# Kernel tuning notes

Hardware: AMD Instinct MI355X
Metric: run time of the kernel (lower is better)

## Reference

```python
import jax, jax.numpy as jnp
import numpy as np

B, NPG, DEG, D, OUT = 256, 256, 16, 128, 12  # graphs, nodes/graph, avg degree, width, out dim
N = B * NPG
E = N * DEG
K = NPG // 2  # TopKPooling ratio 0.5
BN_EPS = 1e-5


def setup_inputs() -> dict:
    key = jax.random.key(0)
    ks = jax.random.split(key, 12)
    x = jax.random.randint(ks[0], (N, 9), 0, 128)
    # within-graph random edges
    local = jax.random.randint(ks[1], (2, B, NPG * DEG), 0, NPG)
    edge_index = (local + (jnp.arange(B) * NPG)[None, :, None]).reshape(2, E)
    edge_attr = jax.random.randint(ks[2], (E, 3), 0, 16)
    batch = jnp.repeat(jnp.arange(B), NPG)
    return {
        "x": x,
        "edge_index": edge_index,
        "edge_attr": edge_attr,
        "batch": batch,
        "atom_emb": jax.random.normal(ks[3], (9, 128, D), jnp.float32) * 0.1,
        "bond_emb": jax.random.normal(ks[4], (3, 16, D), jnp.float32) * 0.1,
        "conv_W": jax.random.normal(ks[5], (5, D, D), jnp.float32) * 0.05,
        "conv_b": jnp.zeros((5, D), jnp.float32),
        "bn_gamma": jnp.ones((5, D), jnp.float32),
        "bn_beta": jnp.zeros((5, D), jnp.float32),
        "eps": jnp.zeros((5,), jnp.float32),  # GINConv train_eps init 0
        "topk_w": jax.random.normal(ks[6], (D,), jnp.float32),
        "out_W": jax.random.normal(ks[7], (D, OUT), jnp.float32) * 0.05,
        "out_b": jnp.zeros((OUT,), jnp.float32),
    }


def _gin(h, src, dst, n_nodes, W, b, g, be, e):
    # sum-aggregate neighbors (dummy segment n_nodes absorbs masked edges)
    agg = jax.ops.segment_sum(h[src], dst, num_segments=n_nodes + 1)[:n_nodes]
    z = ((1.0 + e) * h + agg) @ W + b
    mu = z.mean(0)
    var = ((z - mu) ** 2).mean(0)  # biased var, BatchNorm1d training mode
    z = (z - mu) * jax.lax.rsqrt(var + BN_EPS) * g + be
    return jax.nn.relu(z)


def reference(atom_emb, bond_emb, conv_W, conv_b, bn_gamma, bn_beta, eps,
              topk_w, out_W, out_b, x, edge_index, edge_attr, batch):
    h = atom_emb[jnp.arange(9)[None, :], x].sum(1)  # AtomEncoder: [N, D]
    _eh = bond_emb[jnp.arange(3)[None, :], edge_attr].sum(1)  # BondEncoder (unused by GINConv; DCE'd)
    src, dst = edge_index[0], edge_index[1]

    for layer in range(3):
        h = _gin(h, src, dst, N, conv_W[layer], conv_b[layer],
                 bn_gamma[layer], bn_beta[layer], eps[layer])

    # TopKPooling(ratio=0.5): score = x.w/||w||, keep top half per graph, gate by tanh(score)
    score = h @ topk_w / jnp.linalg.norm(topk_w)  # [N]
    idx_local = jax.lax.top_k(score.reshape(B, NPG), K)[1]  # [B, K]
    perm = (idx_local + (jnp.arange(B) * NPG)[:, None]).reshape(-1)  # [B*K]
    N2 = B * K
    h = h[perm] * jnp.tanh(score[perm])[:, None]
    inv = jnp.full((N,), N2, dtype=jnp.int32).at[perm].set(jnp.arange(N2, dtype=jnp.int32))
    s2, d2 = inv[src], inv[dst]
    valid = (s2 < N2) & (d2 < N2)
    s2 = jnp.where(valid, s2, 0)
    d2 = jnp.where(valid, d2, N2)  # dropped edges -> dummy segment

    for layer in range(3, 5):
        h = _gin(h, s2, d2, N2, conv_W[layer], conv_b[layer],
                 bn_gamma[layer], bn_beta[layer], eps[layer])

    batch2 = batch[perm]  # each graph keeps exactly K nodes
    pooled = jax.ops.segment_sum(h, batch2, num_segments=B) / K  # global_mean_pool
    return jax.nn.sigmoid(pooled @ out_W + out_b)  # [B, OUT]
```

## Files before the change

kernel.cpp:

```cpp
#include <hip/hip_runtime.h>
#include <math.h>

#define NN   65536
#define BB   256
#define NPGC 256
#define EE   1048576
#define DD   128
#define KK   128
#define NT2  32768
#define OUTD 12
#define BN_EPS 1e-5f
#define INV_N1 (1.f / 65536.f)
#define INV_N2 (1.f / 32768.f)

typedef __attribute__((ext_vector_type(8))) short bf16x8;
typedef __attribute__((ext_vector_type(4))) float f32x4;

__device__ __forceinline__ unsigned short bf16_rne(float v) {
    unsigned u = __float_as_uint(v);
    unsigned r = u + 0x7FFFu + ((u >> 16) & 1u);
    return (unsigned short)(r >> 16);
}

__global__ void k_prepw(const float* __restrict__ Wg, unsigned short* __restrict__ wtHi,
                        unsigned short* __restrict__ wtLo) {
    int b = blockIdx.x;
    int l = b >> 7, n = b & 127;
    int k = threadIdx.x;
    float v = Wg[l * 16384 + k * 128 + n];
    unsigned short hb = bf16_rne(v);
    float hf = __uint_as_float((unsigned)hb << 16);
    unsigned short lb = bf16_rne(v - hf);
    wtHi[l * 16384 + n * 128 + k] = hb;
    wtLo[l * 16384 + n * 128 + k] = lb;
}

__device__ __forceinline__ void scan256(int t, const int* in, int* out, int* wtot) {
    int lane = t & 63, w = t >> 6;
    int v = (t < 256) ? in[t] : 0;
    int sv = v;
#pragma unroll
    for (int d = 1; d < 64; d <<= 1) {
        int u = __shfl_up(sv, d);
        if (lane >= d) sv += u;
    }
    if (t < 256 && lane == 63) wtot[w] = sv;
    __syncthreads();
    if (t < 256) {
        int off = 0;
        for (int i = 0; i < w; ++i) off += wtot[i];
        out[t] = sv + off;
    }
    __syncthreads();
}

__global__ __launch_bounds__(1024) void k_mega(
    const int* __restrict__ x, const int* __restrict__ ei,
    const float* __restrict__ emb,
    const unsigned short* __restrict__ wtHi, const unsigned short* __restrict__ wtLo,
    const float* __restrict__ bg, const float* __restrict__ gam,
    const float* __restrict__ bet, const float* __restrict__ epsArr,
    const float* __restrict__ tw, const float* __restrict__ oW,
    const float* __restrict__ ob, float* __restrict__ bnst,
    float* __restrict__ out)
{
    __shared__ __align__(16) unsigned char U[131072];
    __shared__ __align__(16) unsigned short wS[2][4096];
    __shared__ unsigned char csr8[4096];
    __shared__ int offl[257];
    __shared__ int curl[256];
    __shared__ int sscan[256];
    __shared__ int wtot[4];
    __shared__ float score[256];
    __shared__ float scsh[256];
    __shared__ float wlds[128];
    __shared__ float pooled[128];
    __shared__ unsigned char newid[256];
    __shared__ unsigned char perml[128];
    __shared__ unsigned char flg[256];
    __shared__ float invn_s;

    float* hF = (float*)U;
    float2* hF2 = (float2*)U;
    unsigned short* aHi = (unsigned short*)U;
    unsigned short* aLo = (unsigned short*)(U + 65536);
    unsigned* bcnt = (unsigned*)(bnst + 5 * 256);

    const int g = blockIdx.x;
    const int t = threadIdx.x;
    const int wv = t >> 6, l = t & 63;
    const int la = l & 15, kg = l >> 4;
    const int nbase = g * NPGC;
    const int* srcg = ei + g * 4096;
    const int* dstg = ei + EE + g * 4096;

    {
        int* xr = (int*)wS;
        for (int i = t; i < NPGC * 9; i += 1024) xr[i] = x[nbase * 9 + i];
        __syncthreads();
        int n = t >> 2, cq = (t & 3) << 5;
        f32x4 a8[8] = {};
#pragma unroll
        for (int f = 0; f < 9; ++f) {
            const f32x4* ep = (const f32x4*)&emb[(size_t)((f << 7) + xr[n * 9 + f]) * DD + cq];
#pragma unroll
            for (int q = 0; q < 8; ++q) a8[q] += ep[q];
        }
        f32x4* hq = (f32x4*)&hF[n * DD + cq];
#pragma unroll
        for (int q = 0; q < 8; ++q) hq[q] = a8[q];
    }

    for (int i = t; i < 256; i += 1024) curl[i] = 0;
    __syncthreads();
    for (int i = t; i < 4096; i += 1024) atomicAdd(&curl[dstg[i] - nbase], 1);
    __syncthreads();
    scan256(t, curl, sscan, wtot);
    if (t < 256) offl[t] = sscan[t] - curl[t];
    if (t == 0) offl[256] = 4096;
    for (int i = t; i < 256; i += 1024) curl[i] = 0;
    __syncthreads();
    for (int i = t; i < 4096; i += 1024) {
        int d = dstg[i] - nbase;
        int slot = offl[d] + atomicAdd(&curl[d], 1);
        csr8[slot] = (unsigned char)(srcg[i] - nbase);
    }
    __syncthreads();

    for (int L = 0; L < 3; ++L) {
        const float opEps = 1.f + epsArr[L];
        float agx[16], agy[16];
#pragma unroll
        for (int i = 0; i < 16; ++i) {
            int node = wv * 16 + i;
            int st = offl[node], en = offl[node + 1];
            float2 a = hF2[node * 64 + l];
            float ax = a.x * opEps, ay = a.y * opEps;
            int j = st;
            for (; j + 3 < en; j += 4) {
                int n0 = csr8[j], n1 = csr8[j + 1], n2 = csr8[j + 2], n3 = csr8[j + 3];
                float2 v0 = hF2[n0 * 64 + l];
                float2 v1 = hF2[n1 * 64 + l];
                float2 v2 = hF2[n2 * 64 + l];
                float2 v3 = hF2[n3 * 64 + l];
                ax += v0.x + v1.x + v2.x + v3.x;
                ay += v0.y + v1.y + v2.y + v3.y;
            }
            for (; j < en; ++j) {
                float2 v = hF2[csr8[j] * 64 + l];
                ax += v.x; ay += v.y;
            }
            agx[i] = ax; agy[i] = ay;
        }
        __syncthreads();
#pragma unroll
        for (int i = 0; i < 16; ++i) {
            int node = wv * 16 + i;
            int idx = (node * DD + l * 2) ^ ((node & 7) << 3);
            unsigned short hx = bf16_rne(agx[i]);
            unsigned short hy = bf16_rne(agy[i]);
            float rx = agx[i] - __uint_as_float((unsigned)hx << 16);
            float ry = agy[i] - __uint_as_float((unsigned)hy << 16);
            *(unsigned*)&aHi[idx] = (unsigned)hx | ((unsigned)hy << 16);
            *(unsigned*)&aLo[idx] = (unsigned)bf16_rne(rx) | ((unsigned)bf16_rne(ry) << 16);
        }
        const unsigned short* WH = wtHi + L * 16384;
        const unsigned short* WL = wtLo + L * 16384;
        f32x4 acc[8] = {};
        const int rowa = wv * 16 + la;
        const int aXor = (rowa & 7) << 3;
        int e0 = (t & 511) * 8;
        int wn = e0 >> 5, wk = e0 & 31;
        int wdst = e0 ^ (((wn >> 1) & 3) << 3);
        const unsigned short* wbase = (t < 512 ? WH : WL) + wn * 128 + wk;
        bf16x8 wreg = *(const bf16x8*)wbase;
        for (int c = 0; c < 4; ++c) {
            __syncthreads();
            *(bf16x8*)&wS[t >> 9][wdst] = wreg;
            __syncthreads();
            if (c < 3) wreg = *(const bf16x8*)(wbase + (c + 1) * 32);
            int ai = (rowa * DD + c * 32 + kg * 8) ^ aXor;
            bf16x8 ah = *(const bf16x8*)&aHi[ai];
            bf16x8 al = *(const bf16x8*)&aLo[ai];
#pragma unroll
            for (int gi = 0; gi < 8; ++gi) {
                int nn = gi * 16 + la;
                int bi = (nn * 32 + kg * 8) ^ (((nn >> 1) & 3) << 3);
                bf16x8 bh = *(const bf16x8*)&wS[0][bi];
                bf16x8 bl = *(const bf16x8*)&wS[1][bi];
                acc[gi] = __builtin_amdgcn_mfma_f32_16x16x32_bf16(ah, bh, acc[gi], 0, 0, 0);
                acc[gi] = __builtin_amdgcn_mfma_f32_16x16x32_bf16(ah, bl, acc[gi], 0, 0, 0);
                acc[gi] = __builtin_amdgcn_mfma_f32_16x16x32_bf16(al, bh, acc[gi], 0, 0, 0);
            }
        }
        __syncthreads();
        float* partS = (float*)U;
        float* partQ = (float*)(U + 8192);
#pragma unroll
        for (int gi = 0; gi < 8; ++gi) {
            int col = gi * 16 + la;
            float bv = bg[L * DD + col];
            float s = 0.f, q = 0.f;
#pragma unroll
            for (int r = 0; r < 4; ++r) {
                float o = acc[gi][r] + bv;
                acc[gi][r] = o;
                s += o; q += o * o;
            }
            s += __shfl_xor(s, 16); s += __shfl_xor(s, 32);
            q += __shfl_xor(q, 16); q += __shfl_xor(q, 32);
            if (kg == 0) { partS[wv * DD + col] = s; partQ[wv * DD + col] = q; }
        }
        __syncthreads();
        if (t < DD) {
            float s = 0.f, q = 0.f;
#pragma unroll
            for (int i = 0; i < 16; ++i) { s += partS[i * DD + t]; q += partQ[i * DD + t]; }
            atomicAdd(&bnst[L * 256 + t], s);
            atomicAdd(&bnst[L * 256 + DD + t], q);
        }
        __syncthreads();
        if (t == 0) {
            __threadfence();
            atomicAdd(bcnt, 1u);
            unsigned tgt = 256u * (unsigned)(L + 1);
            while (__hip_atomic_load(bcnt, __ATOMIC_RELAXED, __HIP_MEMORY_SCOPE_AGENT) < tgt)
                __builtin_amdgcn_s_sleep(2);
            __threadfence();
        }
        __syncthreads();
        if (t < DD) {
            float s = __hip_atomic_load(&bnst[L * 256 + t], __ATOMIC_RELAXED, __HIP_MEMORY_SCOPE_AGENT);
            float q = __hip_atomic_load(&bnst[L * 256 + DD + t], __ATOMIC_RELAXED, __HIP_MEMORY_SCOPE_AGENT);
            float mu = s * INV_N1;
            float var = q * INV_N1 - mu * mu;
            float istd = rsqrtf(var + BN_EPS);
            float ga = gam[L * DD + t], be = bet[L * DD + t];
            scsh[t] = ga * istd;
            scsh[DD + t] = be - mu * ga * istd;
        }
        __syncthreads();
#pragma unroll
        for (int gi = 0; gi < 8; ++gi) {
            int col = gi * 16 + la;
            float sc = scsh[col], sh = scsh[DD + col];
#pragma unroll
            for (int r = 0; r < 4; ++r) {
                int row = wv * 16 + kg * 4 + r;
                hF[row * DD + col] = fmaxf(acc[gi][r] * sc + sh, 0.f);
            }
        }
        __syncthreads();
    }

    if (t < DD) wlds[t] = tw[t];
    __syncthreads();
    if (t < 64) {
        float s = wlds[t] * wlds[t] + wlds[t + 64] * wlds[t + 64];
#pragma unroll
        for (int d = 32; d > 0; d >>= 1) s += __shfl_down(s, d);
        if (t == 0) invn_s = rsqrtf(s);
    }
    __syncthreads();
    {
        float wx = wlds[l * 2], wy = wlds[l * 2 + 1];
        for (int i = 0; i < 16; ++i) {
            int node = wv * 16 + i;
            float2 a = hF2[node * 64 + l];
            float p = a.x * wx + a.y * wy;
            p += __shfl_xor(p, 32); p += __shfl_xor(p, 16); p += __shfl_xor(p, 8);
            p += __shfl_xor(p, 4);  p += __shfl_xor(p, 2);  p += __shfl_xor(p, 1);
            if (l == 0) score[node] = p * invn_s;
        }
    }
    __syncthreads();
    if (t < 256) {
        float v = score[t];
        int rank = 0;
        for (int j = 0; j < 256; ++j) {
            float u = score[j];
            rank += (u > v) || (u == v && j < t);
        }
        int sel = rank < KK ? 1 : 0;
        flg[t] = (unsigned char)sel;
        sscan[t] = sel;
    }
    __syncthreads();
    scan256(t, sscan, sscan, wtot);
    if (t < 256) {
        if (flg[t]) {
            int m = sscan[t] - 1;
            newid[t] = (unsigned char)m;
            perml[m] = (unsigned char)t;
        } else {
            newid[t] = 0xFF;
        }
    }
    __syncthreads();
    {
        int m = t >> 3, cs = (t & 7) << 4;
        int src = perml[m];
        float tg = tanhf(score[src]);
        f32x4 gv[4];
#pragma unroll
        for (int q = 0; q < 4; ++q) {
            gv[q] = ((const f32x4*)&hF[src * DD + cs])[q];
            gv[q].x *= tg; gv[q].y *= tg; gv[q].z *= tg; gv[q].w *= tg;
        }
        __syncthreads();
#pragma unroll
        for (int q = 0; q < 4; ++q) ((f32x4*)&hF[m * DD + cs])[q] = gv[q];
    }
    __syncthreads();

    for (int i = t; i < 256; i += 1024) curl[i] = 0;
    __syncthreads();
    for (int i = t; i < 4096; i += 1024) {
        int sn = newid[srcg[i] - nbase], dn = newid[dstg[i] - nbase];
        if (sn != 255 && dn != 255) atomicAdd(&curl[dn], 1);
    }
    __syncthreads();
    scan256(t, curl, sscan, wtot);
    if (t < 256) offl[t] = sscan[t] - curl[t];
    for (int i = t; i < 256; i += 1024) curl[i] = 0;
    __syncthreads();
    for (int i = t; i < 4096; i += 1024) {
        int sn = newid[srcg[i] - nbase], dn = newid[dstg[i] - nbase];
        if (sn != 255 && dn != 255) {
            int slot = offl[dn] + atomicAdd(&curl[dn], 1);
            csr8[slot] = (unsigned char)sn;
        }
    }
    __syncthreads();

    unsigned short* aHi2 = (unsigned short*)(U + 65536);
    unsigned short* aLo2 = (unsigned short*)(U + 65536 + 32768);
    for (int L = 3; L < 5; ++L) {
        const float opEps = 1.f + epsArr[L];
        float agx[8], agy[8];
#pragma unroll
        for (int i = 0; i < 8; ++i) {
            int node = wv * 8 + i;
            int st = offl[node], en = offl[node + 1];
            float2 a = hF2[node * 64 + l];
            float ax = a.x * opEps, ay = a.y * opEps;
            int j = st;
            for (; j + 3 < en; j += 4) {
                int n0 = csr8[j], n1 = csr8[j + 1], n2 = csr8[j + 2], n3 = csr8[j + 3];
                float2 v0 = hF2[n0 * 64 + l];
                float2 v1 = hF2[n1 * 64 + l];
                float2 v2 = hF2[n2 * 64 + l];
                float2 v3 = hF2[n3 * 64 + l];
                ax += v0.x + v1.x + v2.x + v3.x;
                ay += v0.y + v1.y + v2.y + v3.y;
            }
            for (; j < en; ++j) {
                float2 v = hF2[csr8[j] * 64 + l];
                ax += v.x; ay += v.y;
            }
            agx[i] = ax; agy[i] = ay;
        }
        __syncthreads();
#pragma unroll
        for (int i = 0; i < 8; ++i) {
            int node = wv * 8 + i;
            int idx = (node * DD + l * 2) ^ ((node & 7) << 3);
            unsigned short hx = bf16_rne(agx[i]);
            unsigned short hy = bf16_rne(agy[i]);
            float rx = agx[i] - __uint_as_float((unsigned)hx << 16);
            float ry = agy[i] - __uint_as_float((unsigned)hy << 16);
            *(unsigned*)&aHi2[idx] = (unsigned)hx | ((unsigned)hy << 16);
            *(unsigned*)&aLo2[idx] = (unsigned)bf16_rne(rx) | ((unsigned)bf16_rne(ry) << 16);
        }
        const unsigned short* WH = wtHi + L * 16384;
        const unsigned short* WL = wtLo + L * 16384;
        f32x4 acc[8] = {};
        const int rowa = wv * 16 + la;
        const int aXor = (rowa & 7) << 3;
        int e0 = (t & 511) * 8;
        int wn = e0 >> 5, wk = e0 & 31;
        int wdst = e0 ^ (((wn >> 1) & 3) << 3);
        const unsigned short* wbase = (t < 512 ? WH : WL) + wn * 128 + wk;
        bf16x8 wreg = *(const bf16x8*)wbase;
        for (int c = 0; c < 4; ++c) {
            __syncthreads();
            *(bf16x8*)&wS[t >> 9][wdst] = wreg;
            __syncthreads();
            if (c < 3) wreg = *(const bf16x8*)(wbase + (c + 1) * 32);
            if (wv < 8) {
                int ai = (rowa * DD + c * 32 + kg * 8) ^ aXor;
                bf16x8 ah = *(const bf16x8*)&aHi2[ai];
                bf16x8 al = *(const bf16x8*)&aLo2[ai];
#pragma unroll
                for (int gi = 0; gi < 8; ++gi) {
                    int nn = gi * 16 + la;
                    int bi = (nn * 32 + kg * 8) ^ (((nn >> 1) & 3) << 3);
                    bf16x8 bh = *(const bf16x8*)&wS[0][bi];
                    bf16x8 bl = *(const bf16x8*)&wS[1][bi];
                    acc[gi] = __builtin_amdgcn_mfma_f32_16x16x32_bf16(ah, bh, acc[gi], 0, 0, 0);
                    acc[gi] = __builtin_amdgcn_mfma_f32_16x16x32_bf16(ah, bl, acc[gi], 0, 0, 0);
                    acc[gi] = __builtin_amdgcn_mfma_f32_16x16x32_bf16(al, bh, acc[gi], 0, 0, 0);
                }
            }
        }
        __syncthreads();
        float* partS = (float*)(U + 65536);
        float* partQ = (float*)(U + 65536 + 4096);
        if (wv < 8) {
#pragma unroll
            for (int gi = 0; gi < 8; ++gi) {
                int col = gi * 16 + la;
                float bv = bg[L * DD + col];
                float s = 0.f, q = 0.f;
#pragma unroll
                for (int r = 0; r < 4; ++r) {
                    float o = acc[gi][r] + bv;
                    acc[gi][r] = o;
                    s += o; q += o * o;
                }
                s += __shfl_xor(s, 16); s += __shfl_xor(s, 32);
                q += __shfl_xor(q, 16); q += __shfl_xor(q, 32);
                if (kg == 0) { partS[wv * 128 + col] = s; partQ[wv * 128 + col] = q; }
            }
        }
        __syncthreads();
        if (t < DD) {
            float s = 0.f, q = 0.f;
#pragma unroll
            for (int i = 0; i < 8; ++i) { s += partS[i * 128 + t]; q += partQ[i * 128 + t]; }
            atomicAdd(&bnst[L * 256 + t], s);
            atomicAdd(&bnst[L * 256 + DD + t], q);
        }
        __syncthreads();
        if (t == 0) {
            __threadfence();
            atomicAdd(bcnt, 1u);
            unsigned tgt = 256u * (unsigned)(L + 1);
            while (__hip_atomic_load(bcnt, __ATOMIC_RELAXED, __HIP_MEMORY_SCOPE_AGENT) < tgt)
                __builtin_amdgcn_s_sleep(2);
            __threadfence();
        }
        __syncthreads();
        if (t < DD) {
            float s = __hip_atomic_load(&bnst[L * 256 + t], __ATOMIC_RELAXED, __HIP_MEMORY_SCOPE_AGENT);
            float q = __hip_atomic_load(&bnst[L * 256 + DD + t], __ATOMIC_RELAXED, __HIP_MEMORY_SCOPE_AGENT);
            float mu = s * INV_N2;
            float var = q * INV_N2 - mu * mu;
            float istd = rsqrtf(var + BN_EPS);
            float ga = gam[L * DD + t], be = bet[L * DD + t];
            scsh[t] = ga * istd;
            scsh[DD + t] = be - mu * ga * istd;
        }
        __syncthreads();
        if (wv < 8) {
#pragma unroll
            for (int gi = 0; gi < 8; ++gi) {
                int col = gi * 16 + la;
                float sc = scsh[col], sh = scsh[DD + col];
#pragma unroll
                for (int r = 0; r < 4; ++r) {
                    int row = wv * 16 + kg * 4 + r;
                    hF[row * DD + col] = fmaxf(acc[gi][r] * sc + sh, 0.f);
                }
            }
        }
        __syncthreads();
    }

    {
        float* partP = (float*)(U + 65536);
        int c = t & 127, grp = t >> 7;
        float s = 0.f;
        for (int r = grp * 16; r < grp * 16 + 16; ++r) s += hF[r * DD + c];
        partP[grp * DD + c] = s;
        float* oWl = (float*)(U + 65536 + 8192);
        for (int i = t; i < DD * OUTD; i += 1024) oWl[i] = oW[i];
        __syncthreads();
        if (t < DD) {
            float s2 = 0.f;
#pragma unroll
            for (int i = 0; i < 8; ++i) s2 += partP[i * DD + t];
            pooled[t] = s2 * (1.f / (float)KK);
        }
        __syncthreads();
        if (t < OUTD) {
            float o = ob[t];
            for (int k = 0; k < DD; ++k) o += pooled[k] * oWl[k * OUTD + t];
            out[g * OUTD + t] = 1.f / (1.f + expf(-o));
        }
    }
}

extern "C" void kernel_launch(void* const* d_in, const int* in_sizes, int n_in,
                              void* d_out, int out_size, void* d_ws, size_t ws_size,
                              hipStream_t stream) {
    const int*   x        = (const int*)d_in[0];
    const int*   ei       = (const int*)d_in[1];
    const float* atom_emb = (const float*)d_in[4];
    const float* convW    = (const float*)d_in[6];
    const float* convb    = (const float*)d_in[7];
    const float* gam      = (const float*)d_in[8];
    const float* bet      = (const float*)d_in[9];
    const float* eps      = (const float*)d_in[10];
    const float* tw       = (const float*)d_in[11];
    const float* oW       = (const float*)d_in[12];
    const float* ob       = (const float*)d_in[13];
    float* outp = (float*)d_out;

    char* p = (char*)d_ws;
    float* bnst = (float*)p;                   p += (size_t)5 * 256 * 4 + 16;
    unsigned short* wtHi = (unsigned short*)p; p += (size_t)5 * DD * DD * 2;
    unsigned short* wtLo = (unsigned short*)p; p += (size_t)5 * DD * DD * 2;
    if ((size_t)(p - (char*)d_ws) > ws_size) return;

    hipMemsetAsync(bnst, 0, (size_t)5 * 256 * 4 + 16, stream);
    k_prepw<<<640, 128, 0, stream>>>(convW, wtHi, wtLo);

    void* args[] = {
        (void*)&x, (void*)&ei, (void*)&atom_emb, (void*)&wtHi, (void*)&wtLo,
        (void*)&convb, (void*)&gam, (void*)&bet, (void*)&eps, (void*)&tw,
        (void*)&oW, (void*)&ob, (void*)&bnst, (void*)&outp
    };
    hipLaunchCooperativeKernel((void*)k_mega, dim3(BB), dim3(1024), args, 0, stream);
}
```

Before: 324.1 us.

## Shard BN stat atomics and barrier counters, pad CSR for packed neighbor gathers

```diff
diff --git a/kernel.cpp b/kernel.cpp
--- a/kernel.cpp
+++ b/kernel.cpp
@@ -61,12 +61,13 @@
     const float* __restrict__ bg, const float* __restrict__ gam,
     const float* __restrict__ bet, const float* __restrict__ epsArr,
     const float* __restrict__ tw, const float* __restrict__ oW,
-    const float* __restrict__ ob, float* __restrict__ bnst,
+    const float* __restrict__ ob, float* __restrict__ bnstP,
+    unsigned* __restrict__ bar, unsigned* __restrict__ rel,
     float* __restrict__ out)
 {
     __shared__ __align__(16) unsigned char U[131072];
     __shared__ __align__(16) unsigned short wS[2][4096];
-    __shared__ unsigned char csr8[4096];
+    __shared__ __align__(4) unsigned char csr8[5120];
     __shared__ int offl[257];
     __shared__ int curl[256];
     __shared__ int sscan[256];
@@ -84,7 +85,6 @@
     float2* hF2 = (float2*)U;
     unsigned short* aHi = (unsigned short*)U;
     unsigned short* aLo = (unsigned short*)(U + 65536);
-    unsigned* bcnt = (unsigned*)(bnst + 5 * 256);
 
     const int g = blockIdx.x;
     const int t = threadIdx.x;
@@ -94,6 +94,8 @@
     const int* srcg = ei + g * 4096;
     const int* dstg = ei + EE + g * 4096;
 
+    const int bucket = g & 7;
+
     {
         int* xr = (int*)wS;
         for (int i = t; i < NPGC * 9; i += 1024) xr[i] = x[nbase * 9 + i];
@@ -115,9 +117,11 @@
     __syncthreads();
     for (int i = t; i < 4096; i += 1024) atomicAdd(&curl[dstg[i] - nbase], 1);
     __syncthreads();
-    scan256(t, curl, sscan, wtot);
-    if (t < 256) offl[t] = sscan[t] - curl[t];
-    if (t == 0) offl[256] = 4096;
+    if (t < 256) sscan[t] = (curl[t] + 3) & ~3;
+    __syncthreads();
+    scan256(t, sscan, sscan, wtot);
+    if (t < 256) offl[t] = sscan[t] - ((curl[t] + 3) & ~3);
+    if (t == 255) offl[256] = sscan[255];
     for (int i = t; i < 256; i += 1024) curl[i] = 0;
     __syncthreads();
     for (int i = t; i < 4096; i += 1024) {
@@ -126,31 +130,52 @@
         csr8[slot] = (unsigned char)(srcg[i] - nbase);
     }
     __syncthreads();
+    if (t < 256) {
+        int cnt = curl[t], st = offl[t], en = offl[t + 1];
+        for (int s2 = cnt; s2 < en - st; ++s2) csr8[st + s2] = (unsigned char)t;
+    }
+    __syncthreads();
 
     for (int L = 0; L < 3; ++L) {
         const float opEps = 1.f + epsArr[L];
         float agx[16], agy[16];
 #pragma unroll
-        for (int i = 0; i < 16; ++i) {
-            int node = wv * 16 + i;
-            int st = offl[node], en = offl[node + 1];
-            float2 a = hF2[node * 64 + l];
-            float ax = a.x * opEps, ay = a.y * opEps;
-            int j = st;
-            for (; j + 3 < en; j += 4) {
-                int n0 = csr8[j], n1 = csr8[j + 1], n2 = csr8[j + 2], n3 = csr8[j + 3];
-                float2 v0 = hF2[n0 * 64 + l];
-                float2 v1 = hF2[n1 * 64 + l];
-                float2 v2 = hF2[n2 * 64 + l];
-                float2 v3 = hF2[n3 * 64 + l];
-                ax += v0.x + v1.x + v2.x + v3.x;
-                ay += v0.y + v1.y + v2.y + v3.y;
-            }
-            for (; j < en; ++j) {
-                float2 v = hF2[csr8[j] * 64 + l];
-                ax += v.x; ay += v.y;
-            }
-            agx[i] = ax; agy[i] = ay;
+        for (int r = 0; r < 8; ++r) {
+            int n0 = wv * 16 + r * 2, n1 = n0 + 1;
+            int s0 = offl[n0], e0 = offl[n0 + 1];
+            int s1 = offl[n1], e1 = offl[n1 + 1];
+            int p0 = (e0 - s0) - curl[n0];
+            int p1 = (e1 - s1) - curl[n1];
+            float2 a0 = hF2[n0 * 64 + l], a1 = hF2[n1 * 64 + l];
+            float acx0 = a0.x * (opEps - (float)p0), acy0 = a0.y * (opEps - (float)p0);
+            float acx1 = a1.x * (opEps - (float)p1), acy1 = a1.y * (opEps - (float)p1);
+            int mA = (e0 - s0) >> 2, mB = (e1 - s1) >> 2;
+            int mx = mA > mB ? mA : mB;
+            unsigned pkA = (mA > 0) ? *(const unsigned*)&csr8[s0] : 0u;
+            unsigned pkB = (mB > 0) ? *(const unsigned*)&csr8[s1] : 0u;
+            for (int k = 0; k < mx; ++k) {
+                unsigned cA = pkA, cB = pkB;
+                if (k + 1 < mA) pkA = *(const unsigned*)&csr8[s0 + ((k + 1) << 2)];
+                if (k + 1 < mB) pkB = *(const unsigned*)&csr8[s1 + ((k + 1) << 2)];
+                if (k < mA) {
+                    float2 v0 = hF2[(cA & 255u) * 64 + l];
+                    float2 v1 = hF2[((cA >> 8) & 255u) * 64 + l];
+                    float2 v2 = hF2[((cA >> 16) & 255u) * 64 + l];
+                    float2 v3 = hF2[(cA >> 24) * 64 + l];
+                    acx0 += v0.x + v1.x + v2.x + v3.x;
+                    acy0 += v0.y + v1.y + v2.y + v3.y;
+                }
+                if (k < mB) {
+                    float2 v0 = hF2[(cB & 255u) * 64 + l];
+                    float2 v1 = hF2[((cB >> 8) & 255u) * 64 + l];
+                    float2 v2 = hF2[((cB >> 16) & 255u) * 64 + l];
+                    float2 v3 = hF2[(cB >> 24) * 64 + l];
+                    acx1 += v0.x + v1.x + v2.x + v3.x;
+                    acy1 += v0.y + v1.y + v2.y + v3.y;
+                }
+            }
+            agx[r * 2] = acx0; agy[r * 2] = acy0;
+            agx[r * 2 + 1] = acx1; agy[r * 2 + 1] = acy1;
         }
         __syncthreads();
 #pragma unroll
@@ -169,9 +194,9 @@
         f32x4 acc[8] = {};
         const int rowa = wv * 16 + la;
         const int aXor = (rowa & 7) << 3;
-        int e0 = (t & 511) * 8;
-        int wn = e0 >> 5, wk = e0 & 31;
-        int wdst = e0 ^ (((wn >> 1) & 3) << 3);
+        int e0w = (t & 511) * 8;
+        int wn = e0w >> 5, wk = e0w & 31;
+        int wdst = e0w ^ (((wn >> 1) & 3) << 3);
         const unsigned short* wbase = (t < 512 ? WH : WL) + wn * 128 + wk;
         bf16x8 wreg = *(const bf16x8*)wbase;
         for (int c = 0; c < 4; ++c) {
@@ -212,26 +237,45 @@
             if (kg == 0) { partS[wv * DD + col] = s; partQ[wv * DD + col] = q; }
         }
         __syncthreads();
+        float* bnstL = bnstP + L * 2048 + bucket * 256;
         if (t < DD) {
             float s = 0.f, q = 0.f;
 #pragma unroll
             for (int i = 0; i < 16; ++i) { s += partS[i * DD + t]; q += partQ[i * DD + t]; }
-            atomicAdd(&bnst[L * 256 + t], s);
-            atomicAdd(&bnst[L * 256 + DD + t], q);
+            atomicAdd(&bnstL[t], s);
+            atomicAdd(&bnstL[DD + t], q);
         }
         __syncthreads();
         if (t == 0) {
             __threadfence();
-            atomicAdd(bcnt, 1u);
+            atomicAdd(&bar[bucket * 64], 1u);
             unsigned tgt = 256u * (unsigned)(L + 1);
-            while (__hip_atomic_load(bcnt, __ATOMIC_RELAXED, __HIP_MEMORY_SCOPE_AGENT) < tgt)
-                __builtin_amdgcn_s_sleep(2);
-            __threadfence();
+            if (g == 0) {
+                unsigned tot;
+                do {
+                    tot = 0;
+#pragma unroll
+                    for (int b = 0; b < 8; ++b)
+                        tot += __hip_atomic_load(&bar[b * 64], __ATOMIC_RELAXED, __HIP_MEMORY_SCOPE_AGENT);
+                    if (tot < tgt) __builtin_amdgcn_s_sleep(1);
+                } while (tot < tgt);
+                __threadfence();
+                __hip_atomic_store(rel, (unsigned)(L + 1), __ATOMIC_RELEASE, __HIP_MEMORY_SCOPE_AGENT);
+            } else {
+                while (__hip_atomic_load(rel, __ATOMIC_ACQUIRE, __HIP_MEMORY_SCOPE_AGENT) < (unsigned)(L + 1))
+                    __builtin_amdgcn_s_sleep(1);
+                __threadfence();
+            }
         }
         __syncthreads();
         if (t < DD) {
-            float s = __hip_atomic_load(&bnst[L * 256 + t], __ATOMIC_RELAXED, __HIP_MEMORY_SCOPE_AGENT);
-            float q = __hip_atomic_load(&bnst[L * 256 + DD + t], __ATOMIC_RELAXED, __HIP_MEMORY_SCOPE_AGENT);
+            float s = 0.f, q = 0.f;
+            const float* bp = bnstP + L * 2048;
+#pragma unroll
+            for (int b = 0; b < 8; ++b) {
+                s += __hip_atomic_load(&bp[b * 256 + t], __ATOMIC_RELAXED, __HIP_MEMORY_SCOPE_AGENT);
+                q += __hip_atomic_load(&bp[b * 256 + DD + t], __ATOMIC_RELAXED, __HIP_MEMORY_SCOPE_AGENT);
+            }
             float mu = s * INV_N1;
             float var = q * INV_N1 - mu * mu;
             float istd = rsqrtf(var + BN_EPS);
@@ -320,8 +364,11 @@
         if (sn != 255 && dn != 255) atomicAdd(&curl[dn], 1);
     }
     __syncthreads();
-    scan256(t, curl, sscan, wtot);
-    if (t < 256) offl[t] = sscan[t] - curl[t];
+    if (t < 256) sscan[t] = (curl[t] + 3) & ~3;
+    __syncthreads();
+    scan256(t, sscan, sscan, wtot);
+    if (t < 256) offl[t] = sscan[t] - ((curl[t] + 3) & ~3);
+    if (t == 255) offl[256] = sscan[255];
     for (int i = t; i < 256; i += 1024) curl[i] = 0;
     __syncthreads();
     for (int i = t; i < 4096; i += 1024) {
@@ -332,6 +379,11 @@
         }
     }
     __syncthreads();
+    if (t < 128) {
+        int cnt = curl[t], st = offl[t], en = offl[t + 1];
+        for (int s2 = cnt; s2 < en - st; ++s2) csr8[st + s2] = (unsigned char)t;
+    }
+    __syncthreads();
 
     unsigned short* aHi2 = (unsigned short*)(U + 65536);
     unsigned short* aLo2 = (unsigned short*)(U + 65536 + 32768);
@@ -339,26 +391,42 @@
         const float opEps = 1.f + epsArr[L];
         float agx[8], agy[8];
 #pragma unroll
-        for (int i = 0; i < 8; ++i) {
-            int node = wv * 8 + i;
-            int st = offl[node], en = offl[node + 1];
-            float2 a = hF2[node * 64 + l];
-            float ax = a.x * opEps, ay = a.y * opEps;
-            int j = st;
-            for (; j + 3 < en; j += 4) {
-                int n0 = csr8[j], n1 = csr8[j + 1], n2 = csr8[j + 2], n3 = csr8[j + 3];
-                float2 v0 = hF2[n0 * 64 + l];
-                float2 v1 = hF2[n1 * 64 + l];
-                float2 v2 = hF2[n2 * 64 + l];
-                float2 v3 = hF2[n3 * 64 + l];
-                ax += v0.x + v1.x + v2.x + v3.x;
-                ay += v0.y + v1.y + v2.y + v3.y;
-            }
-            for (; j < en; ++j) {
-                float2 v = hF2[csr8[j] * 64 + l];
-                ax += v.x; ay += v.y;
-            }
-            agx[i] = ax; agy[i] = ay;
+        for (int r = 0; r < 4; ++r) {
+            int n0 = wv * 8 + r * 2, n1 = n0 + 1;
+            int s0 = offl[n0], e0 = offl[n0 + 1];
+            int s1 = offl[n1], e1 = offl[n1 + 1];
+            int p0 = (e0 - s0) - curl[n0];
+            int p1 = (e1 - s1) - curl[n1];
+            float2 a0 = hF2[n0 * 64 + l], a1 = hF2[n1 * 64 + l];
+            float acx0 = a0.x * (opEps - (float)p0), acy0 = a0.y * (opEps - (float)p0);
+            float acx1 = a1.x * (opEps - (float)p1), acy1 = a1.y * (opEps - (float)p1);
+            int mA = (e0 - s0) >> 2, mB = (e1 - s1) >> 2;
+            int mx = mA > mB ? mA : mB;
+            unsigned pkA = (mA > 0) ? *(const unsigned*)&csr8[s0] : 0u;
+            unsigned pkB = (mB > 0) ? *(const unsigned*)&csr8[s1] : 0u;
+            for (int k = 0; k < mx; ++k) {
+                unsigned cA = pkA, cB = pkB;
+                if (k + 1 < mA) pkA = *(const unsigned*)&csr8[s0 + ((k + 1) << 2)];
+                if (k + 1 < mB) pkB = *(const unsigned*)&csr8[s1 + ((k + 1) << 2)];
+                if (k < mA) {
+                    float2 v0 = hF2[(cA & 255u) * 64 + l];
+                    float2 v1 = hF2[((cA >> 8) & 255u) * 64 + l];
+                    float2 v2 = hF2[((cA >> 16) & 255u) * 64 + l];
+                    float2 v3 = hF2[(cA >> 24) * 64 + l];
+                    acx0 += v0.x + v1.x + v2.x + v3.x;
+                    acy0 += v0.y + v1.y + v2.y + v3.y;
+                }
+                if (k < mB) {
+                    float2 v0 = hF2[(cB & 255u) * 64 + l];
+                    float2 v1 = hF2[((cB >> 8) & 255u) * 64 + l];
+                    float2 v2 = hF2[((cB >> 16) & 255u) * 64 + l];
+                    float2 v3 = hF2[(cB >> 24) * 64 + l];
+                    acx1 += v0.x + v1.x + v2.x + v3.x;
+                    acy1 += v0.y + v1.y + v2.y + v3.y;
+                }
+            }
+            agx[r * 2] = acx0; agy[r * 2] = acy0;
+            agx[r * 2 + 1] = acx1; agy[r * 2 + 1] = acy1;
         }
         __syncthreads();
 #pragma unroll
@@ -377,9 +445,9 @@
         f32x4 acc[8] = {};
         const int rowa = wv * 16 + la;
         const int aXor = (rowa & 7) << 3;
-        int e0 = (t & 511) * 8;
-        int wn = e0 >> 5, wk = e0 & 31;
-        int wdst = e0 ^ (((wn >> 1) & 3) << 3);
+        int e0w = (t & 511) * 8;
+        int wn = e0w >> 5, wk = e0w & 31;
+        int wdst = e0w ^ (((wn >> 1) & 3) << 3);
         const unsigned short* wbase = (t < 512 ? WH : WL) + wn * 128 + wk;
         bf16x8 wreg = *(const bf16x8*)wbase;
         for (int c = 0; c < 4; ++c) {
@@ -424,26 +492,45 @@
             }
         }
         __syncthreads();
+        float* bnstL = bnstP + L * 2048 + bucket * 256;
         if (t < DD) {
             float s = 0.f, q = 0.f;
 #pragma unroll
             for (int i = 0; i < 8; ++i) { s += partS[i * 128 + t]; q += partQ[i * 128 + t]; }
-            atomicAdd(&bnst[L * 256 + t], s);
-            atomicAdd(&bnst[L * 256 + DD + t], q);
+            atomicAdd(&bnstL[t], s);
+            atomicAdd(&bnstL[DD + t], q);
         }
         __syncthreads();
         if (t == 0) {
             __threadfence();
-            atomicAdd(bcnt, 1u);
+            atomicAdd(&bar[bucket * 64], 1u);
             unsigned tgt = 256u * (unsigned)(L + 1);
-            while (__hip_atomic_load(bcnt, __ATOMIC_RELAXED, __HIP_MEMORY_SCOPE_AGENT) < tgt)
-                __builtin_amdgcn_s_sleep(2);
-            __threadfence();
+            if (g == 0) {
+                unsigned tot;
+                do {
+                    tot = 0;
+#pragma unroll
+                    for (int b = 0; b < 8; ++b)
+                        tot += __hip_atomic_load(&bar[b * 64], __ATOMIC_RELAXED, __HIP_MEMORY_SCOPE_AGENT);
+                    if (tot < tgt) __builtin_amdgcn_s_sleep(1);
+                } while (tot < tgt);
+                __threadfence();
+                __hip_atomic_store(rel, (unsigned)(L + 1), __ATOMIC_RELEASE, __HIP_MEMORY_SCOPE_AGENT);
+            } else {
+                while (__hip_atomic_load(rel, __ATOMIC_ACQUIRE, __HIP_MEMORY_SCOPE_AGENT) < (unsigned)(L + 1))
+                    __builtin_amdgcn_s_sleep(1);
+                __threadfence();
+            }
         }
         __syncthreads();
         if (t < DD) {
-            float s = __hip_atomic_load(&bnst[L * 256 + t], __ATOMIC_RELAXED, __HIP_MEMORY_SCOPE_AGENT);
-            float q = __hip_atomic_load(&bnst[L * 256 + DD + t], __ATOMIC_RELAXED, __HIP_MEMORY_SCOPE_AGENT);
+            float s = 0.f, q = 0.f;
+            const float* bp = bnstP + L * 2048;
+#pragma unroll
+            for (int b = 0; b < 8; ++b) {
+                s += __hip_atomic_load(&bp[b * 256 + t], __ATOMIC_RELAXED, __HIP_MEMORY_SCOPE_AGENT);
+                q += __hip_atomic_load(&bp[b * 256 + DD + t], __ATOMIC_RELAXED, __HIP_MEMORY_SCOPE_AGENT);
+            }
             float mu = s * INV_N2;
             float var = q * INV_N2 - mu * mu;
             float istd = rsqrtf(var + BN_EPS);
@@ -508,18 +595,20 @@
     float* outp = (float*)d_out;
 
     char* p = (char*)d_ws;
-    float* bnst = (float*)p;                   p += (size_t)5 * 256 * 4 + 16;
+    float* bnstP = (float*)p;                  p += (size_t)5 * 8 * 256 * 4;
+    unsigned* bar = (unsigned*)p;              p += (size_t)8 * 64 * 4;
+    unsigned* rel = (unsigned*)p;              p += 256;
     unsigned short* wtHi = (unsigned short*)p; p += (size_t)5 * DD * DD * 2;
     unsigned short* wtLo = (unsigned short*)p; p += (size_t)5 * DD * DD * 2;
     if ((size_t)(p - (char*)d_ws) > ws_size) return;
 
-    hipMemsetAsync(bnst, 0, (size_t)5 * 256 * 4 + 16, stream);
+    hipMemsetAsync(bnstP, 0, (size_t)5 * 8 * 256 * 4 + 8 * 64 * 4 + 256, stream);
     k_prepw<<<640, 128, 0, stream>>>(convW, wtHi, wtLo);
 
     void* args[] = {
         (void*)&x, (void*)&ei, (void*)&atom_emb, (void*)&wtHi, (void*)&wtLo,
         (void*)&convb, (void*)&gam, (void*)&bet, (void*)&eps, (void*)&tw,
-        (void*)&oW, (void*)&ob, (void*)&bnst, (void*)&outp
+        (void*)&oW, (void*)&ob, (void*)&bnstP, (void*)&bar, (void*)&rel, (void*)&outp
     };
     hipLaunchCooperativeKernel((void*)k_mega, dim3(BB), dim3(1024), args, 0, stream);
 }
```

New measurement: 366.4 us. 1.13x slower.
